# Optimization experiments

Measured on AMD Instinct MI355X. Metric: run time of the kernel, lower is better.

## Reference

```python
import jax, jax.numpy as jnp
import numpy as np

N = 50000   # nodes
E = 800000  # edges
F = 128     # num_features
H = 128     # hidden_size


def gcn_conv(x, W, b, src, dst, num_nodes):
    """PyG-style GCNConv: x' = D^{-1/2}(A+I)D^{-1/2} (x @ W) + b."""
    xw = x @ W  # [N, H] transform before propagation (PyG order)
    # add self loops
    loop = jnp.arange(num_nodes)
    s = jnp.concatenate([src, loop])
    d = jnp.concatenate([dst, loop])
    # symmetric normalization: degree counted on target nodes
    deg = jax.ops.segment_sum(jnp.ones(s.shape[0], dtype=xw.dtype), d,
                              num_segments=num_nodes)
    dinv = jnp.where(deg > 0, jax.lax.rsqrt(deg), 0.0)
    norm = dinv[s] * dinv[d]            # [E+N]
    msgs = xw[s] * norm[:, None]        # gather + scale
    out = jax.ops.segment_sum(msgs, d, num_segments=num_nodes)  # scatter-add
    return out + b


def setup_inputs() -> dict:
    key = jax.random.key(0)
    ks = jax.random.split(key, 6)
    x = jax.random.normal(ks[0], (N, F), dtype=jnp.float32)
    edge_index = jax.random.randint(ks[1], (2, E), 0, N, dtype=jnp.int32)
    W1 = jax.random.normal(ks[2], (F, H), dtype=jnp.float32) * (1.0 / np.sqrt(F))
    b1 = jnp.zeros((H,), dtype=jnp.float32)
    W2 = jax.random.normal(ks[3], (H, H), dtype=jnp.float32) * (1.0 / np.sqrt(H))
    b2 = jnp.zeros((H,), dtype=jnp.float32)
    Wf = jax.random.normal(ks[4], (H, 1), dtype=jnp.float32) * (1.0 / np.sqrt(H))
    bf = jnp.zeros((1,), dtype=jnp.float32)
    return {"x": x, "edge_index": edge_index, "W1": W1, "b1": b1,
            "W2": W2, "b2": b2, "Wf": Wf, "bf": bf}


def reference(x, edge_index, W1, b1, W2, b2, Wf, bf):
    src, dst = edge_index[0], edge_index[1]
    h = jax.nn.relu(gcn_conv(x, W1, b1, src, dst, N))
    h = jax.nn.relu(gcn_conv(h, W2, b2, src, dst, N))
    return (h @ Wf + bf)[:, 0]  # [N]
```

## Files before the change

### kernel.cpp

```cpp
#include <hip/hip_runtime.h>
#include <hip/hip_bf16.h>


#define FDIM 128
#define BSHIFT 8
#define BNODES 256
#define MAXB 256
#define CHUNK 2048
#define CAP 5120

typedef unsigned int uint;
typedef unsigned short ushort;
typedef __attribute__((ext_vector_type(8))) short short8v;
typedef __attribute__((ext_vector_type(4))) float f32x4;

__device__ inline float2 bf2f(uint u) {
    return make_float2(__uint_as_float(u << 16), __uint_as_float(u & 0xffff0000u));
}
__device__ inline ushort f2bf(float f) {
    uint u = __float_as_uint(f);
    return (ushort)((u + 0x7fffu + ((u >> 16) & 1u)) >> 16);
}
__device__ inline float bfval(ushort h) { return __uint_as_float((uint)h << 16); }
__device__ inline uint packbf2(float a, float b) {
    return (uint)f2bf(a) | ((uint)f2bf(b) << 16);
}
__device__ inline int swz(int row, int colShorts) {
    return (((colShorts >> 3) ^ (row & 7)) << 3) | (colShorts & 7);
}

template <int CHAINS, bool SCALE>
__device__ __forceinline__ void gemm_core(int bid, const void* __restrict__ Xv,
                                          const float* __restrict__ W,
                                          const float* __restrict__ dinv,
                                          ushort* __restrict__ Y, int M,
                                          ushort (*Xh)[64], ushort (*Xl)[64],
                                          ushort (*Wth)[64], ushort (*Wtl)[64]) {
    const int t = threadIdx.x;
    const int wv = t >> 6;
    const int lane = t & 63;
    const int rb = bid * 64;

    f32x4 acc[8];
    #pragma unroll
    for (int i = 0; i < 8; ++i) acc[i] = (f32x4){0.f, 0.f, 0.f, 0.f};

    for (int kc = 0; kc < 2; ++kc) {
        const int k0 = kc * 64;
        if constexpr (CHAINS == 3) {
            const float* Xf = (const float*)Xv;
            #pragma unroll
            for (int it = 0; it < 4; ++it) {
                int idx = t + it * 256;
                int r = idx >> 4, c4 = (idx & 15) * 4;
                int gr = rb + r;
                float4 v = make_float4(0.f, 0.f, 0.f, 0.f);
                if (gr < M) v = *(const float4*)&Xf[(size_t)gr * FDIM + k0 + c4];
                ushort h0 = f2bf(v.x), h1 = f2bf(v.y), h2 = f2bf(v.z), h3 = f2bf(v.w);
                uint2 hw, lw;
                hw.x = (uint)h0 | ((uint)h1 << 16);
                hw.y = (uint)h2 | ((uint)h3 << 16);
                lw.x = (uint)f2bf(v.x - bfval(h0)) | ((uint)f2bf(v.y - bfval(h1)) << 16);
                lw.y = (uint)f2bf(v.z - bfval(h2)) | ((uint)f2bf(v.w - bfval(h3)) << 16);
                int cs = swz(r, c4);
                *(uint2*)&Xh[r][cs] = hw;
                *(uint2*)&Xl[r][cs] = lw;
            }
        } else {
            const ushort* Xb = (const ushort*)Xv;
            #pragma unroll
            for (int it = 0; it < 4; ++it) {
                int idx = t + it * 256;
                int r = idx >> 4, c4 = (idx & 15) * 4;
                int gr = rb + r;
                uint2 u = make_uint2(0u, 0u);
                if (gr < M) u = *(const uint2*)&Xb[(size_t)gr * FDIM + k0 + c4];
                *(uint2*)&Xh[r][swz(r, c4)] = u;
            }
        }
        {
            int n = t & 127, kk0 = (t >> 7) * 32;
            #pragma unroll
            for (int g = 0; g < 4; ++g) {
                uint hw[4], lw[4];
                #pragma unroll
                for (int jp = 0; jp < 4; ++jp) {
                    int k = k0 + kk0 + g * 8 + jp * 2;
                    float w0 = W[(size_t)k * FDIM + n];
                    float w1 = W[(size_t)(k + 1) * FDIM + n];
                    ushort h0 = f2bf(w0), h1 = f2bf(w1);
                    hw[jp] = (uint)h0 | ((uint)h1 << 16);
                    lw[jp] = (uint)f2bf(w0 - bfval(h0)) | ((uint)f2bf(w1 - bfval(h1)) << 16);
                }
                int cs = swz(n, kk0 + g * 8);
                *(uint4*)&Wth[n][cs] = make_uint4(hw[0], hw[1], hw[2], hw[3]);
                *(uint4*)&Wtl[n][cs] = make_uint4(lw[0], lw[1], lw[2], lw[3]);
            }
        }
        __syncthreads();
        const int arow = 16 * wv + (lane & 15);
        #pragma unroll
        for (int ks = 0; ks < 2; ++ks) {
            const int kf = ks * 32 + ((lane >> 4) << 3);
            short8v ah = *(const short8v*)&Xh[arow][swz(arow, kf)];
            short8v al;
            if constexpr (CHAINS == 3) al = *(const short8v*)&Xl[arow][swz(arow, kf)];
            #pragma unroll
            for (int ct = 0; ct < 8; ++ct) {
                int brow = 16 * ct + (lane & 15);
                int bcs = swz(brow, kf);
                short8v bh = *(const short8v*)&Wth[brow][bcs];
                short8v bl = *(const short8v*)&Wtl[brow][bcs];
                acc[ct] = __builtin_amdgcn_mfma_f32_16x16x32_bf16(ah, bh, acc[ct], 0, 0, 0);
                acc[ct] = __builtin_amdgcn_mfma_f32_16x16x32_bf16(ah, bl, acc[ct], 0, 0, 0);
                if constexpr (CHAINS == 3)
                    acc[ct] = __builtin_amdgcn_mfma_f32_16x16x32_bf16(al, bh, acc[ct], 0, 0, 0);
            }
        }
        __syncthreads();
    }
    const int rbase = rb + 16 * wv + ((lane >> 4) << 2);
    const int cbase = lane & 15;
    #pragma unroll
    for (int ri = 0; ri < 4; ++ri) {
        int R = rbase + ri;
        if (R < M) {
            float s = SCALE ? dinv[R] : 1.0f;
            ushort* Yrow = Y + (size_t)R * FDIM;
            #pragma unroll
            for (int ct = 0; ct < 8; ++ct)
                Yrow[16 * ct + cbase] = f2bf(acc[ct][ri] * s);
        }
    }
}

__global__ __launch_bounds__(256) void k_scat_gemm(const int* __restrict__ src,
                                                   const int* __restrict__ dst,
                                                   int* __restrict__ bincnt,
                                                   uint* __restrict__ binbuf, int E, int nwg,
                                                   const void* __restrict__ Xv,
                                                   const float* __restrict__ W,
                                                   ushort* __restrict__ Y, int M) {
    __shared__ alignas(16) ushort Xh[64][64];
    __shared__ alignas(16) ushort Xl[64][64];
    __shared__ alignas(16) ushort Wth[128][64];
    __shared__ alignas(16) ushort Wtl[128][64];
    __shared__ int h[MAXB], base[MAXB], cnt[MAXB];

    if (blockIdx.x >= nwg) {
        gemm_core<3, false>(blockIdx.x - nwg, Xv, W, nullptr, Y, M, Xh, Xl, Wth, Wtl);
        return;
    }
    int t = threadIdx.x;
    h[t] = 0;
    cnt[t] = 0;
    __syncthreads();
    int b0 = blockIdx.x * CHUNK;
    #pragma unroll
    for (int i = 0; i < CHUNK / 256; ++i) {
        int e = b0 + i * 256 + t;
        if (e < E) atomicAdd(&h[dst[e] >> BSHIFT], 1);
    }
    __syncthreads();
    if (h[t]) base[t] = atomicAdd(&bincnt[t], h[t]);
    __syncthreads();
    #pragma unroll
    for (int i = 0; i < CHUNK / 256; ++i) {
        int e = b0 + i * 256 + t;
        if (e < E) {
            int d = dst[e];
            int b = d >> BSHIFT;
            int r = atomicAdd(&cnt[b], 1);
            binbuf[(size_t)b * CAP + base[b] + r] = (uint)(((d - (b << BSHIFT)) << 16) | src[e]);
        }
    }
}

template <int CHAINS, bool SCALE>
__global__ __launch_bounds__(256) void k_gemm_mfma(const void* __restrict__ Xv,
                                                   const float* __restrict__ W,
                                                   const float* __restrict__ dinv,
                                                   ushort* __restrict__ Y, int M) {
    __shared__ alignas(16) ushort Xh[64][64];
    __shared__ alignas(16) ushort Xl[(CHAINS == 3) ? 64 : 1][64];
    __shared__ alignas(16) ushort Wth[128][64];
    __shared__ alignas(16) ushort Wtl[128][64];
    gemm_core<CHAINS, SCALE>(blockIdx.x, Xv, W, dinv, Y, M, Xh, Xl, Wth, Wtl);
}

__global__ __launch_bounds__(BNODES) void k_bucket(const uint* __restrict__ binbuf,
                                                   const int* __restrict__ bincnt,
                                                   int* __restrict__ row_ptr,
                                                   int* __restrict__ degO,
                                                   float* __restrict__ dinv,
                                                   int* __restrict__ col, int N) {
    __shared__ int sdeg[BNODES], sexcl[BNODES], scnt[BNODES];
    int b = blockIdx.x, t = threadIdx.x;
    int gnode = (b << BSHIFT) + t;
    sdeg[t] = 0;
    scnt[t] = 0;
    __syncthreads();
    int beg = b * CAP, count = bincnt[b];
    for (int i = t; i < count; i += BNODES)
        atomicAdd(&sdeg[binbuf[beg + i] >> 16], 1);
    __syncthreads();
    int d = sdeg[t];
    sexcl[t] = d;
    __syncthreads();
    for (int off = 1; off < BNODES; off <<= 1) {
        int u = (t >= off) ? sexcl[t - off] : 0;
        __syncthreads();
        sexcl[t] += u;
        __syncthreads();
    }
    int excl = sexcl[t] - d;
    if (gnode < N) {
        row_ptr[gnode] = beg + excl;
        degO[gnode] = d;
        dinv[gnode] = rsqrtf((float)d + 1.0f);
    }
    __syncthreads();
    sexcl[t] = excl;
    __syncthreads();
    for (int i = t; i < count; i += BNODES) {
        uint p = binbuf[beg + i];
        int dl = p >> 16;
        int r = atomicAdd(&scnt[dl], 1);
        col[beg + sexcl[dl] + r] = (int)(p & 0xffffu);
    }
}

template <bool SCALE_EDGES, bool FINAL>
__global__ __launch_bounds__(256) void k_agg(const uint* __restrict__ y,
                                             const float* __restrict__ bvec,
                                             const float* __restrict__ dinv,
                                             const int* __restrict__ row_ptr,
                                             const int* __restrict__ degA,
                                             const int* __restrict__ col,
                                             uint* __restrict__ h,
                                             const float* __restrict__ Wf,
                                             const float* __restrict__ bfp,
                                             float* __restrict__ out, int n) {
    int wid = threadIdx.x >> 6, lane = threadIdx.x & 63;
    int node = blockIdx.x * 4 + wid;
    if (node >= n) return;
    int beg = row_ptr[node], end = beg + degA[node];
    float dn = dinv[node];
    float2 acc = bf2f(y[(size_t)node * 64 + lane]);
    if (SCALE_EDGES) { acc.x *= dn; acc.y *= dn; }
    int e = beg;
    for (; e + 8 <= end; e += 8) {
        int s0 = col[e],     s1 = col[e + 1], s2 = col[e + 2], s3 = col[e + 3];
        int s4 = col[e + 4], s5 = col[e + 5], s6 = col[e + 6], s7 = col[e + 7];
        uint v0 = y[(size_t)s0 * 64 + lane];
        uint v1 = y[(size_t)s1 * 64 + lane];
        uint v2 = y[(size_t)s2 * 64 + lane];
        uint v3 = y[(size_t)s3 * 64 + lane];
        uint v4 = y[(size_t)s4 * 64 + lane];
        uint v5 = y[(size_t)s5 * 64 + lane];
        uint v6 = y[(size_t)s6 * 64 + lane];
        uint v7 = y[(size_t)s7 * 64 + lane];
        float2 f0 = bf2f(v0), f1 = bf2f(v1), f2 = bf2f(v2), f3 = bf2f(v3);
        float2 f4 = bf2f(v4), f5 = bf2f(v5), f6 = bf2f(v6), f7 = bf2f(v7);
        if (SCALE_EDGES) {
            float d0 = dinv[s0], d1 = dinv[s1], d2 = dinv[s2], d3 = dinv[s3];
            float d4 = dinv[s4], d5 = dinv[s5], d6 = dinv[s6], d7 = dinv[s7];
            acc.x = fmaf(f0.x, d0, acc.x); acc.y = fmaf(f0.y, d0, acc.y);
            acc.x = fmaf(f1.x, d1, acc.x); acc.y = fmaf(f1.y, d1, acc.y);
            acc.x = fmaf(f2.x, d2, acc.x); acc.y = fmaf(f2.y, d2, acc.y);
            acc.x = fmaf(f3.x, d3, acc.x); acc.y = fmaf(f3.y, d3, acc.y);
            acc.x = fmaf(f4.x, d4, acc.x); acc.y = fmaf(f4.y, d4, acc.y);
            acc.x = fmaf(f5.x, d5, acc.x); acc.y = fmaf(f5.y, d5, acc.y);
            acc.x = fmaf(f6.x, d6, acc.x); acc.y = fmaf(f6.y, d6, acc.y);
            acc.x = fmaf(f7.x, d7, acc.x); acc.y = fmaf(f7.y, d7, acc.y);
        } else {
            acc.x += ((f0.x + f1.x) + (f2.x + f3.x)) + ((f4.x + f5.x) + (f6.x + f7.x));
            acc.y += ((f0.y + f1.y) + (f2.y + f3.y)) + ((f4.y + f5.y) + (f6.y + f7.y));
        }
    }
    for (; e < end; ++e) {
        int s = col[e];
        float2 f = bf2f(y[(size_t)s * 64 + lane]);
        if (SCALE_EDGES) {
            float ds = dinv[s];
            acc.x = fmaf(f.x, ds, acc.x);
            acc.y = fmaf(f.y, ds, acc.y);
        } else {
            acc.x += f.x;
            acc.y += f.y;
        }
    }
    float2 bb = *(const float2*)&bvec[lane * 2];
    float ox = fmaxf(fmaf(acc.x, dn, bb.x), 0.f);
    float oy = fmaxf(fmaf(acc.y, dn, bb.y), 0.f);
    if (FINAL) {
        float2 wf = *(const float2*)&Wf[lane * 2];
        float s = ox * wf.x + oy * wf.y;
        #pragma unroll
        for (int off = 32; off > 0; off >>= 1) s += __shfl_xor(s, off);
        if (lane == 0) out[node] = s + bfp[0];
    } else {
        h[(size_t)node * 64 + lane] = packbf2(ox, oy);
    }
}


extern "C" void kernel_launch(void* const* d_in, const int* in_sizes, int n_in,
                              void* d_out, int out_size, void* d_ws, size_t ws_size,
                              hipStream_t stream) {
    const float* x  = (const float*)d_in[0];
    const int*   ei = (const int*)d_in[1];
    const float* W1 = (const float*)d_in[2];
    const float* b1 = (const float*)d_in[3];
    const float* W2 = (const float*)d_in[4];
    const float* b2 = (const float*)d_in[5];
    const float* Wf = (const float*)d_in[6];
    const float* bf = (const float*)d_in[7];

    const int N = in_sizes[0] / FDIM;
    const int E = in_sizes[1] / 2;
    const int* src = ei;
    const int* dst = ei + E;
    const int nb = (N + BNODES - 1) >> BSHIFT;

    char* ws = (char*)d_ws;
    size_t off = 0;
    auto alloc = [&](size_t bytes) -> void* {
        void* p = ws + off;
        off = (off + bytes + 511) & ~(size_t)511;
        return p;
    };
    uint*  bufA    = (uint*)alloc((size_t)N * FDIM * 2);
    uint*  bufB    = (uint*)alloc((size_t)N * FDIM * 2);
    int*   col     = (int*)alloc((size_t)nb * CAP * 4);
    uint*  binbuf  = (uint*)alloc((size_t)nb * CAP * 4);
    float* dinv    = (float*)alloc((size_t)N * 4);
    int*   row_ptr = (int*)alloc((size_t)N * 4);
    int*   deg     = (int*)alloc((size_t)N * 4);
    int*   bincnt  = (int*)alloc(MAXB * 4);

    hipMemsetAsync(bincnt, 0, MAXB * 4, stream);

    const int nwg = (E + CHUNK - 1) / CHUNK;
    const int gb  = (N + 63) / 64;
    k_scat_gemm<<<nwg + gb, 256, 0, stream>>>(src, dst, bincnt, binbuf, E, nwg,
                                              x, W1, (ushort*)bufA, N);
    k_bucket<<<nb, BNODES, 0, stream>>>(binbuf, bincnt, row_ptr, deg, dinv, col, N);

    k_agg<true, false><<<(N + 3) / 4, 256, 0, stream>>>(bufA, b1, dinv, row_ptr, deg, col,
                                                        bufB, nullptr, nullptr, nullptr, N);
    k_gemm_mfma<2, true><<<gb, 256, 0, stream>>>(bufB, W2, dinv, (ushort*)bufA, N);
    k_agg<false, true><<<(N + 3) / 4, 256, 0, stream>>>(bufA, b2, dinv, row_ptr, deg, col,
                                                        nullptr, Wf, bf, (float*)d_out, N);
}
```

Measured before the change: 212.1 us.

## Fuse layer-1 aggregation with layer-2 MFMA GEMM and pad bin counters

Merges the first aggregation kernel and the second GEMM into one 512-thread kernel. Each block aggregates 64 nodes into an LDS tile, then multiplies that tile by W2 (split into bf16 hi/lo) with MFMA, which avoids writing and re-reading the intermediate hidden buffer and removes a launch. The per-bin atomic counters are also padded to separate cache lines to reduce contention. The risks are lower occupancy, since each wave serially aggregates 8 nodes before the GEMM, and the W2 conversion being repeated in every block.

```diff
diff --git a/kernel.cpp b/kernel.cpp
--- a/kernel.cpp
+++ b/kernel.cpp
@@ -6,6 +6,7 @@
 #define BSHIFT 8
 #define BNODES 256
 #define MAXB 256
+#define BPAD 16
 #define CHUNK 2048
 #define CAP 5120
 
@@ -162,7 +163,7 @@
         if (e < E) atomicAdd(&h[dst[e] >> BSHIFT], 1);
     }
     __syncthreads();
-    if (h[t]) base[t] = atomicAdd(&bincnt[t], h[t]);
+    if (h[t]) base[t] = atomicAdd(&bincnt[t * BPAD], h[t]);
     __syncthreads();
     #pragma unroll
     for (int i = 0; i < CHUNK / 256; ++i) {
@@ -174,18 +175,6 @@
             binbuf[(size_t)b * CAP + base[b] + r] = (uint)(((d - (b << BSHIFT)) << 16) | src[e]);
         }
     }
-}
-
-template <int CHAINS, bool SCALE>
-__global__ __launch_bounds__(256) void k_gemm_mfma(const void* __restrict__ Xv,
-                                                   const float* __restrict__ W,
-                                                   const float* __restrict__ dinv,
-                                                   ushort* __restrict__ Y, int M) {
-    __shared__ alignas(16) ushort Xh[64][64];
-    __shared__ alignas(16) ushort Xl[(CHAINS == 3) ? 64 : 1][64];
-    __shared__ alignas(16) ushort Wth[128][64];
-    __shared__ alignas(16) ushort Wtl[128][64];
-    gemm_core<CHAINS, SCALE>(blockIdx.x, Xv, W, dinv, Y, M, Xh, Xl, Wth, Wtl);
 }
 
 __global__ __launch_bounds__(BNODES) void k_bucket(const uint* __restrict__ binbuf,
@@ -200,7 +189,7 @@
     sdeg[t] = 0;
     scnt[t] = 0;
     __syncthreads();
-    int beg = b * CAP, count = bincnt[b];
+    int beg = b * CAP, count = bincnt[b * BPAD];
     for (int i = t; i < count; i += BNODES)
         atomicAdd(&sdeg[binbuf[beg + i] >> 16], 1);
     __syncthreads();
@@ -230,24 +219,151 @@
     }
 }
 
-template <bool SCALE_EDGES, bool FINAL>
-__global__ __launch_bounds__(256) void k_agg(const uint* __restrict__ y,
-                                             const float* __restrict__ bvec,
-                                             const float* __restrict__ dinv,
-                                             const int* __restrict__ row_ptr,
-                                             const int* __restrict__ degA,
-                                             const int* __restrict__ col,
-                                             uint* __restrict__ h,
-                                             const float* __restrict__ Wf,
-                                             const float* __restrict__ bfp,
-                                             float* __restrict__ out, int n) {
+__global__ __launch_bounds__(512) void k_agg_gemm(const uint* __restrict__ y,
+                                                  const float* __restrict__ bvec,
+                                                  const float* __restrict__ dinv,
+                                                  const int* __restrict__ row_ptr,
+                                                  const int* __restrict__ degA,
+                                                  const int* __restrict__ col,
+                                                  const float* __restrict__ W,
+                                                  ushort* __restrict__ Y, int N) {
+    __shared__ alignas(16) ushort A[64][128];
+    __shared__ alignas(16) ushort Wth[128][64];
+    __shared__ alignas(16) ushort Wtl[128][64];
+
+    const int t = threadIdx.x;
+    const int wv = t >> 6;
+    const int lane = t & 63;
+    const int rb = blockIdx.x * 64;
+
+    #pragma unroll 1
+    for (int i = 0; i < 8; ++i) {
+        int r = (wv << 3) + i;
+        int node = rb + r;
+        uint packed = 0u;
+        if (node < N) {
+            int beg = row_ptr[node], end = beg + degA[node];
+            float dn = dinv[node];
+            float2 acc = bf2f(y[(size_t)node * 64 + lane]);
+            acc.x *= dn; acc.y *= dn;
+            int e = beg;
+            for (; e + 8 <= end; e += 8) {
+                int s0 = col[e],     s1 = col[e + 1], s2 = col[e + 2], s3 = col[e + 3];
+                int s4 = col[e + 4], s5 = col[e + 5], s6 = col[e + 6], s7 = col[e + 7];
+                uint v0 = y[(size_t)s0 * 64 + lane];
+                uint v1 = y[(size_t)s1 * 64 + lane];
+                uint v2 = y[(size_t)s2 * 64 + lane];
+                uint v3 = y[(size_t)s3 * 64 + lane];
+                uint v4 = y[(size_t)s4 * 64 + lane];
+                uint v5 = y[(size_t)s5 * 64 + lane];
+                uint v6 = y[(size_t)s6 * 64 + lane];
+                uint v7 = y[(size_t)s7 * 64 + lane];
+                float d0 = dinv[s0], d1 = dinv[s1], d2 = dinv[s2], d3 = dinv[s3];
+                float d4 = dinv[s4], d5 = dinv[s5], d6 = dinv[s6], d7 = dinv[s7];
+                float2 f0 = bf2f(v0), f1 = bf2f(v1), f2 = bf2f(v2), f3 = bf2f(v3);
+                float2 f4 = bf2f(v4), f5 = bf2f(v5), f6 = bf2f(v6), f7 = bf2f(v7);
+                acc.x = fmaf(f0.x, d0, acc.x); acc.y = fmaf(f0.y, d0, acc.y);
+                acc.x = fmaf(f1.x, d1, acc.x); acc.y = fmaf(f1.y, d1, acc.y);
+                acc.x = fmaf(f2.x, d2, acc.x); acc.y = fmaf(f2.y, d2, acc.y);
+                acc.x = fmaf(f3.x, d3, acc.x); acc.y = fmaf(f3.y, d3, acc.y);
+                acc.x = fmaf(f4.x, d4, acc.x); acc.y = fmaf(f4.y, d4, acc.y);
+                acc.x = fmaf(f5.x, d5, acc.x); acc.y = fmaf(f5.y, d5, acc.y);
+                acc.x = fmaf(f6.x, d6, acc.x); acc.y = fmaf(f6.y, d6, acc.y);
+                acc.x = fmaf(f7.x, d7, acc.x); acc.y = fmaf(f7.y, d7, acc.y);
+            }
+            for (; e < end; ++e) {
+                int s = col[e];
+                float2 f = bf2f(y[(size_t)s * 64 + lane]);
+                float ds = dinv[s];
+                acc.x = fmaf(f.x, ds, acc.x);
+                acc.y = fmaf(f.y, ds, acc.y);
+            }
+            float2 bb = *(const float2*)&bvec[lane * 2];
+            float ox = fmaxf(fmaf(acc.x, dn, bb.x), 0.f);
+            float oy = fmaxf(fmaf(acc.y, dn, bb.y), 0.f);
+            packed = packbf2(ox, oy);
+        }
+        *(uint*)&A[r][swz(r, 2 * lane)] = packed;
+    }
+    __syncthreads();
+
+    const int rstrip = wv >> 1;
+    const int chalf = wv & 1;
+    f32x4 acc[4];
+    #pragma unroll
+    for (int i = 0; i < 4; ++i) acc[i] = (f32x4){0.f, 0.f, 0.f, 0.f};
+
+    for (int kc = 0; kc < 2; ++kc) {
+        const int k0 = kc * 64;
+        {
+            int n = t & 127, g2 = t >> 7;
+            #pragma unroll
+            for (int gg = 0; gg < 2; ++gg) {
+                int g = g2 + 4 * gg;
+                uint hw[4], lw[4];
+                #pragma unroll
+                for (int jp = 0; jp < 4; ++jp) {
+                    int k = k0 + g * 8 + jp * 2;
+                    float w0 = W[(size_t)k * FDIM + n];
+                    float w1 = W[(size_t)(k + 1) * FDIM + n];
+                    ushort h0 = f2bf(w0), h1 = f2bf(w1);
+                    hw[jp] = (uint)h0 | ((uint)h1 << 16);
+                    lw[jp] = (uint)f2bf(w0 - bfval(h0)) | ((uint)f2bf(w1 - bfval(h1)) << 16);
+                }
+                int cs = swz(n, g * 8);
+                *(uint4*)&Wth[n][cs] = make_uint4(hw[0], hw[1], hw[2], hw[3]);
+                *(uint4*)&Wtl[n][cs] = make_uint4(lw[0], lw[1], lw[2], lw[3]);
+            }
+        }
+        __syncthreads();
+        const int arow = 16 * rstrip + (lane & 15);
+        #pragma unroll
+        for (int ks = 0; ks < 2; ++ks) {
+            const int kf = ks * 32 + ((lane >> 4) << 3);
+            short8v ah = *(const short8v*)&A[arow][swz(arow, k0 + kf)];
+            #pragma unroll
+            for (int c = 0; c < 4; ++c) {
+                int ct = 4 * chalf + c;
+                int brow = 16 * ct + (lane & 15);
+                int bcs = swz(brow, kf);
+                short8v bh = *(const short8v*)&Wth[brow][bcs];
+                short8v bl = *(const short8v*)&Wtl[brow][bcs];
+                acc[c] = __builtin_amdgcn_mfma_f32_16x16x32_bf16(ah, bh, acc[c], 0, 0, 0);
+                acc[c] = __builtin_amdgcn_mfma_f32_16x16x32_bf16(ah, bl, acc[c], 0, 0, 0);
+            }
+        }
+        __syncthreads();
+    }
+    const int rbase = rb + 16 * rstrip + ((lane >> 4) << 2);
+    const int cbase = lane & 15;
+    #pragma unroll
+    for (int ri = 0; ri < 4; ++ri) {
+        int R = rbase + ri;
+        if (R < N) {
+            float s = dinv[R];
+            ushort* Yrow = Y + (size_t)R * FDIM;
+            #pragma unroll
+            for (int c = 0; c < 4; ++c)
+                Yrow[16 * (4 * chalf + c) + cbase] = f2bf(acc[c][ri] * s);
+        }
+    }
+}
+
+__global__ __launch_bounds__(256) void k_agg_final(const uint* __restrict__ y,
+                                                   const float* __restrict__ bvec,
+                                                   const float* __restrict__ dinv,
+                                                   const int* __restrict__ row_ptr,
+                                                   const int* __restrict__ degA,
+                                                   const int* __restrict__ col,
+                                                   const float* __restrict__ Wf,
+                                                   const float* __restrict__ bfp,
+                                                   float* __restrict__ out, int n) {
     int wid = threadIdx.x >> 6, lane = threadIdx.x & 63;
     int node = blockIdx.x * 4 + wid;
     if (node >= n) return;
     int beg = row_ptr[node], end = beg + degA[node];
     float dn = dinv[node];
     float2 acc = bf2f(y[(size_t)node * 64 + lane]);
-    if (SCALE_EDGES) { acc.x *= dn; acc.y *= dn; }
     int e = beg;
     for (; e + 8 <= end; e += 8) {
         int s0 = col[e],     s1 = col[e + 1], s2 = col[e + 2], s3 = col[e + 3];
@@ -262,46 +378,22 @@
         uint v7 = y[(size_t)s7 * 64 + lane];
         float2 f0 = bf2f(v0), f1 = bf2f(v1), f2 = bf2f(v2), f3 = bf2f(v3);
         float2 f4 = bf2f(v4), f5 = bf2f(v5), f6 = bf2f(v6), f7 = bf2f(v7);
-        if (SCALE_EDGES) {
-            float d0 = dinv[s0], d1 = dinv[s1], d2 = dinv[s2], d3 = dinv[s3];
-            float d4 = dinv[s4], d5 = dinv[s5], d6 = dinv[s6], d7 = dinv[s7];
-            acc.x = fmaf(f0.x, d0, acc.x); acc.y = fmaf(f0.y, d0, acc.y);
-            acc.x = fmaf(f1.x, d1, acc.x); acc.y = fmaf(f1.y, d1, acc.y);
-            acc.x = fmaf(f2.x, d2, acc.x); acc.y = fmaf(f2.y, d2, acc.y);
-            acc.x = fmaf(f3.x, d3, acc.x); acc.y = fmaf(f3.y, d3, acc.y);
-            acc.x = fmaf(f4.x, d4, acc.x); acc.y = fmaf(f4.y, d4, acc.y);
-            acc.x = fmaf(f5.x, d5, acc.x); acc.y = fmaf(f5.y, d5, acc.y);
-            acc.x = fmaf(f6.x, d6, acc.x); acc.y = fmaf(f6.y, d6, acc.y);
-            acc.x = fmaf(f7.x, d7, acc.x); acc.y = fmaf(f7.y, d7, acc.y);
-        } else {
-            acc.x += ((f0.x + f1.x) + (f2.x + f3.x)) + ((f4.x + f5.x) + (f6.x + f7.x));
-            acc.y += ((f0.y + f1.y) + (f2.y + f3.y)) + ((f4.y + f5.y) + (f6.y + f7.y));
-        }
+        acc.x += ((f0.x + f1.x) + (f2.x + f3.x)) + ((f4.x + f5.x) + (f6.x + f7.x));
+        acc.y += ((f0.y + f1.y) + (f2.y + f3.y)) + ((f4.y + f5.y) + (f6.y + f7.y));
     }
     for (; e < end; ++e) {
-        int s = col[e];
-        float2 f = bf2f(y[(size_t)s * 64 + lane]);
-        if (SCALE_EDGES) {
-            float ds = dinv[s];
-            acc.x = fmaf(f.x, ds, acc.x);
-            acc.y = fmaf(f.y, ds, acc.y);
-        } else {
-            acc.x += f.x;
-            acc.y += f.y;
-        }
+        float2 f = bf2f(y[(size_t)col[e] * 64 + lane]);
+        acc.x += f.x;
+        acc.y += f.y;
     }
     float2 bb = *(const float2*)&bvec[lane * 2];
     float ox = fmaxf(fmaf(acc.x, dn, bb.x), 0.f);
     float oy = fmaxf(fmaf(acc.y, dn, bb.y), 0.f);
-    if (FINAL) {
-        float2 wf = *(const float2*)&Wf[lane * 2];
-        float s = ox * wf.x + oy * wf.y;
-        #pragma unroll
-        for (int off = 32; off > 0; off >>= 1) s += __shfl_xor(s, off);
-        if (lane == 0) out[node] = s + bfp[0];
-    } else {
-        h[(size_t)node * 64 + lane] = packbf2(ox, oy);
-    }
+    float2 wf = *(const float2*)&Wf[lane * 2];
+    float s = ox * wf.x + oy * wf.y;
+    #pragma unroll
+    for (int off = 32; off > 0; off >>= 1) s += __shfl_xor(s, off);
+    if (lane == 0) out[node] = s + bfp[0];
 }
 
 
@@ -337,9 +429,9 @@
     float* dinv    = (float*)alloc((size_t)N * 4);
     int*   row_ptr = (int*)alloc((size_t)N * 4);
     int*   deg     = (int*)alloc((size_t)N * 4);
-    int*   bincnt  = (int*)alloc(MAXB * 4);
-
-    hipMemsetAsync(bincnt, 0, MAXB * 4, stream);
+    int*   bincnt  = (int*)alloc(MAXB * BPAD * 4);
+
+    hipMemsetAsync(bincnt, 0, MAXB * BPAD * 4, stream);
 
     const int nwg = (E + CHUNK - 1) / CHUNK;
     const int gb  = (N + 63) / 64;
@@ -347,9 +439,8 @@
                                               x, W1, (ushort*)bufA, N);
     k_bucket<<<nb, BNODES, 0, stream>>>(binbuf, bincnt, row_ptr, deg, dinv, col, N);
 
-    k_agg<true, false><<<(N + 3) / 4, 256, 0, stream>>>(bufA, b1, dinv, row_ptr, deg, col,
-                                                        bufB, nullptr, nullptr, nullptr, N);
-    k_gemm_mfma<2, true><<<gb, 256, 0, stream>>>(bufB, W2, dinv, (ushort*)bufA, N);
-    k_agg<false, true><<<(N + 3) / 4, 256, 0, stream>>>(bufA, b2, dinv, row_ptr, deg, col,
-                                                        nullptr, Wf, bf, (float*)d_out, N);
-}
+    k_agg_gemm<<<gb, 512, 0, stream>>>(bufA, b1, dinv, row_ptr, deg, col,
+                                       W2, (ushort*)bufB, N);
+    k_agg_final<<<(N + 3) / 4, 256, 0, stream>>>(bufB, b2, dinv, row_ptr, deg, col,
+                                                 Wf, bf, (float*)d_out, N);
+}
```

Measured after the change: 239.2 us. 1.13x slower.

## Split aggregation across feature slices so each block gathers narrow columns

Applied to the files above, without the earlier changes.

The aggregation kernels now assign each block a 16-lane feature slice (of 4 slices) over 128 nodes, with four edges processed in parallel per wave and reduced via shuffles, so each block's gathered working set is a narrow column slice that may fit better in cache. The final layer accumulates partial dot products into the output with atomics, which requires zeroing the output first. Bin counters are also padded to separate cache lines to reduce atomic contention. In exchange each edge index and dinv value is loaded once per feature slice, each gather moves only 64 bytes, lanes idle when degree is not a multiple of four, and float atomics make the final sum order nondeterministic.

```diff
diff --git a/kernel.cpp b/kernel.cpp
--- a/kernel.cpp
+++ b/kernel.cpp
@@ -6,6 +6,7 @@
 #define BSHIFT 8
 #define BNODES 256
 #define MAXB 256
+#define BPAD 16
 #define CHUNK 2048
 #define CAP 5120
 
@@ -162,7 +163,7 @@
         if (e < E) atomicAdd(&h[dst[e] >> BSHIFT], 1);
     }
     __syncthreads();
-    if (h[t]) base[t] = atomicAdd(&bincnt[t], h[t]);
+    if (h[t]) base[t] = atomicAdd(&bincnt[t * BPAD], h[t]);
     __syncthreads();
     #pragma unroll
     for (int i = 0; i < CHUNK / 256; ++i) {
@@ -200,7 +201,7 @@
     sdeg[t] = 0;
     scnt[t] = 0;
     __syncthreads();
-    int beg = b * CAP, count = bincnt[b];
+    int beg = b * CAP, count = bincnt[b * BPAD];
     for (int i = t; i < count; i += BNODES)
         atomicAdd(&sdeg[binbuf[beg + i] >> 16], 1);
     __syncthreads();
@@ -231,76 +232,70 @@
 }
 
 template <bool SCALE_EDGES, bool FINAL>
-__global__ __launch_bounds__(256) void k_agg(const uint* __restrict__ y,
-                                             const float* __restrict__ bvec,
-                                             const float* __restrict__ dinv,
-                                             const int* __restrict__ row_ptr,
-                                             const int* __restrict__ degA,
-                                             const int* __restrict__ col,
-                                             uint* __restrict__ h,
-                                             const float* __restrict__ Wf,
-                                             const float* __restrict__ bfp,
-                                             float* __restrict__ out, int n) {
-    int wid = threadIdx.x >> 6, lane = threadIdx.x & 63;
-    int node = blockIdx.x * 4 + wid;
-    if (node >= n) return;
-    int beg = row_ptr[node], end = beg + degA[node];
-    float dn = dinv[node];
-    float2 acc = bf2f(y[(size_t)node * 64 + lane]);
-    if (SCALE_EDGES) { acc.x *= dn; acc.y *= dn; }
-    int e = beg;
-    for (; e + 8 <= end; e += 8) {
-        int s0 = col[e],     s1 = col[e + 1], s2 = col[e + 2], s3 = col[e + 3];
-        int s4 = col[e + 4], s5 = col[e + 5], s6 = col[e + 6], s7 = col[e + 7];
-        uint v0 = y[(size_t)s0 * 64 + lane];
-        uint v1 = y[(size_t)s1 * 64 + lane];
-        uint v2 = y[(size_t)s2 * 64 + lane];
-        uint v3 = y[(size_t)s3 * 64 + lane];
-        uint v4 = y[(size_t)s4 * 64 + lane];
-        uint v5 = y[(size_t)s5 * 64 + lane];
-        uint v6 = y[(size_t)s6 * 64 + lane];
-        uint v7 = y[(size_t)s7 * 64 + lane];
-        float2 f0 = bf2f(v0), f1 = bf2f(v1), f2 = bf2f(v2), f3 = bf2f(v3);
-        float2 f4 = bf2f(v4), f5 = bf2f(v5), f6 = bf2f(v6), f7 = bf2f(v7);
+__global__ __launch_bounds__(256) void k_agg_feat(const uint* __restrict__ y,
+                                                  const float* __restrict__ bvec,
+                                                  const float* __restrict__ dinv,
+                                                  const int* __restrict__ row_ptr,
+                                                  const int* __restrict__ degA,
+                                                  const int* __restrict__ col,
+                                                  uint* __restrict__ h,
+                                                  const float* __restrict__ Wf,
+                                                  const float* __restrict__ bfp,
+                                                  float* __restrict__ out, int N) {
+    const int b = blockIdx.x;
+    const int chunk = b >> 3, slot = b & 7;
+    const int g = slot >> 1, half = slot & 1;
+    const int t = threadIdx.x, wv = t >> 6, lane = t & 63;
+    const int fi = (g << 4) + (lane & 15);
+    const int q = lane >> 4;
+    const int base = (chunk << 8) + (half << 7) + (wv << 5);
+
+    for (int i = 0; i < 32; ++i) {
+        int node = base + i;
+        if (node >= N) return;
+        int beg = row_ptr[node];
+        int dg = degA[node];
+        float dn = dinv[node];
+        float2 acc = make_float2(0.f, 0.f);
+        for (int ee = 0; ee < dg; ee += 4) {
+            int idx = ee + q;
+            bool v = idx < dg;
+            int s = v ? col[beg + idx] : 0;
+            uint u = v ? y[(size_t)s * 64 + fi] : 0u;
+            float2 f = bf2f(u);
+            if (SCALE_EDGES) {
+                float ds = v ? dinv[s] : 0.f;
+                acc.x = fmaf(f.x, ds, acc.x);
+                acc.y = fmaf(f.y, ds, acc.y);
+            } else {
+                acc.x += f.x;
+                acc.y += f.y;
+            }
+        }
+        acc.x += __shfl_xor(acc.x, 16); acc.y += __shfl_xor(acc.y, 16);
+        acc.x += __shfl_xor(acc.x, 32); acc.y += __shfl_xor(acc.y, 32);
+        float2 fs = bf2f(y[(size_t)node * 64 + fi]);
         if (SCALE_EDGES) {
-            float d0 = dinv[s0], d1 = dinv[s1], d2 = dinv[s2], d3 = dinv[s3];
-            float d4 = dinv[s4], d5 = dinv[s5], d6 = dinv[s6], d7 = dinv[s7];
-            acc.x = fmaf(f0.x, d0, acc.x); acc.y = fmaf(f0.y, d0, acc.y);
-            acc.x = fmaf(f1.x, d1, acc.x); acc.y = fmaf(f1.y, d1, acc.y);
-            acc.x = fmaf(f2.x, d2, acc.x); acc.y = fmaf(f2.y, d2, acc.y);
-            acc.x = fmaf(f3.x, d3, acc.x); acc.y = fmaf(f3.y, d3, acc.y);
-            acc.x = fmaf(f4.x, d4, acc.x); acc.y = fmaf(f4.y, d4, acc.y);
-            acc.x = fmaf(f5.x, d5, acc.x); acc.y = fmaf(f5.y, d5, acc.y);
-            acc.x = fmaf(f6.x, d6, acc.x); acc.y = fmaf(f6.y, d6, acc.y);
-            acc.x = fmaf(f7.x, d7, acc.x); acc.y = fmaf(f7.y, d7, acc.y);
+            acc.x = fmaf(fs.x, dn, acc.x);
+            acc.y = fmaf(fs.y, dn, acc.y);
         } else {
-            acc.x += ((f0.x + f1.x) + (f2.x + f3.x)) + ((f4.x + f5.x) + (f6.x + f7.x));
-            acc.y += ((f0.y + f1.y) + (f2.y + f3.y)) + ((f4.y + f5.y) + (f6.y + f7.y));
-        }
-    }
-    for (; e < end; ++e) {
-        int s = col[e];
-        float2 f = bf2f(y[(size_t)s * 64 + lane]);
-        if (SCALE_EDGES) {
-            float ds = dinv[s];
-            acc.x = fmaf(f.x, ds, acc.x);
-            acc.y = fmaf(f.y, ds, acc.y);
+            acc.x += fs.x;
+            acc.y += fs.y;
+        }
+        float2 bb = *(const float2*)&bvec[2 * fi];
+        float ox = fmaxf(fmaf(acc.x, dn, bb.x), 0.f);
+        float oy = fmaxf(fmaf(acc.y, dn, bb.y), 0.f);
+        if (FINAL) {
+            float2 wf = *(const float2*)&Wf[2 * fi];
+            float p = ox * wf.x + oy * wf.y;
+            p += __shfl_xor(p, 1);
+            p += __shfl_xor(p, 2);
+            p += __shfl_xor(p, 4);
+            p += __shfl_xor(p, 8);
+            if (lane == 0) atomicAdd(&out[node], p + (slot == 0 ? bfp[0] : 0.f));
         } else {
-            acc.x += f.x;
-            acc.y += f.y;
-        }
-    }
-    float2 bb = *(const float2*)&bvec[lane * 2];
-    float ox = fmaxf(fmaf(acc.x, dn, bb.x), 0.f);
-    float oy = fmaxf(fmaf(acc.y, dn, bb.y), 0.f);
-    if (FINAL) {
-        float2 wf = *(const float2*)&Wf[lane * 2];
-        float s = ox * wf.x + oy * wf.y;
-        #pragma unroll
-        for (int off = 32; off > 0; off >>= 1) s += __shfl_xor(s, off);
-        if (lane == 0) out[node] = s + bfp[0];
-    } else {
-        h[(size_t)node * 64 + lane] = packbf2(ox, oy);
+            if (lane < 16) h[(size_t)node * 64 + fi] = packbf2(ox, oy);
+        }
     }
 }
 
@@ -337,19 +332,22 @@
     float* dinv    = (float*)alloc((size_t)N * 4);
     int*   row_ptr = (int*)alloc((size_t)N * 4);
     int*   deg     = (int*)alloc((size_t)N * 4);
-    int*   bincnt  = (int*)alloc(MAXB * 4);
-
-    hipMemsetAsync(bincnt, 0, MAXB * 4, stream);
+    int*   bincnt  = (int*)alloc(MAXB * BPAD * 4);
+
+    hipMemsetAsync(bincnt, 0, MAXB * BPAD * 4, stream);
+    hipMemsetAsync(d_out, 0, (size_t)out_size * 4, stream);
 
     const int nwg = (E + CHUNK - 1) / CHUNK;
     const int gb  = (N + 63) / 64;
+    const int ab  = ((N + 255) >> 8) * 8;
+
     k_scat_gemm<<<nwg + gb, 256, 0, stream>>>(src, dst, bincnt, binbuf, E, nwg,
                                               x, W1, (ushort*)bufA, N);
     k_bucket<<<nb, BNODES, 0, stream>>>(binbuf, bincnt, row_ptr, deg, dinv, col, N);
 
-    k_agg<true, false><<<(N + 3) / 4, 256, 0, stream>>>(bufA, b1, dinv, row_ptr, deg, col,
-                                                        bufB, nullptr, nullptr, nullptr, N);
+    k_agg_feat<true, false><<<ab, 256, 0, stream>>>(bufA, b1, dinv, row_ptr, deg, col,
+                                                    bufB, nullptr, nullptr, nullptr, N);
     k_gemm_mfma<2, true><<<gb, 256, 0, stream>>>(bufB, W2, dinv, (ushort*)bufA, N);
-    k_agg<false, true><<<(N + 3) / 4, 256, 0, stream>>>(bufA, b2, dinv, row_ptr, deg, col,
-                                                        nullptr, Wf, bf, (float*)d_out, N);
-}
+    k_agg_feat<false, true><<<ab, 256, 0, stream>>>(bufA, b2, dinv, row_ptr, deg, col,
+                                                    nullptr, Wf, bf, (float*)d_out, N);
+}
```

New measurement: 408.7 us. 92.6% more time.
